# Optimization experiments

Hardware: AMD Instinct MI355X
Metric: run time of the kernel (lower is better)

The kernel has to match this reference:

```python
import jax, jax.numpy as jnp
import numpy as np

# Intersection(mode='product'):
#   a_fk = a @ feats.T            # [Na, K]
#   b_fk = b @ feats.T            # [Nb, K]
#   mask = (a_fk[:,None,:] > 0) & (b_fk[None,:,:] > 0)
#   result = sum_k (a_fk[:,None,:] * b_fk[None,:,:]) * mask   # [Na, Nb]
# For the product op, (x*y)*[x>0 & y>0] == relu(x)*relu(y) elementwise
# (any term with a non-positive factor is zeroed either way), so the
# broadcast+mask+reduce collapses exactly into a GEMM over relu'd scores.

def setup_inputs() -> dict:
    key = jax.random.key(0)
    k1, k2, k3 = jax.random.split(key, 3)
    a = jax.random.normal(k1, (1024, 2048), dtype=jnp.float32)
    b = jax.random.normal(k2, (1024, 2048), dtype=jnp.float32)
    feats = jax.random.normal(k3, (128, 2048), dtype=jnp.float32)
    return {"a": a, "b": b, "feats": feats}

def reference(a, b, feats):
    a_fk = a @ feats.T            # [Na, K]
    b_fk = b @ feats.T            # [Nb, K]
    # masked product-intersection reduced over K; identical math to the
    # broadcast (Na, Nb, K) -> sum formulation of the torch module.
    return jnp.einsum('ak,bk->ab', jax.nn.relu(a_fk), jax.nn.relu(b_fk))
```

## Files before the change

kernel.cpp:

```cpp
#include <hip/hip_runtime.h>


typedef __attribute__((ext_vector_type(8))) __bf16 bf16x8;
typedef __attribute__((ext_vector_type(4))) float floatx4;

#define KD     2048
#define NF     128
#define NA     1024
#define NPART  16

static __device__ inline bf16x8 cvt8(float4 u, float4 v) {
    bf16x8 s;
    s[0] = (__bf16)u.x; s[1] = (__bf16)u.y; s[2] = (__bf16)u.z; s[3] = (__bf16)u.w;
    s[4] = (__bf16)v.x; s[5] = (__bf16)v.y; s[6] = (__bf16)v.z; s[7] = (__bf16)v.w;
    return s;
}

static __device__ inline bf16x8 cvt8r(float4 u, float4 v) {
    bf16x8 s;
    s[0] = (__bf16)fmaxf(u.x, 0.f); s[1] = (__bf16)fmaxf(u.y, 0.f);
    s[2] = (__bf16)fmaxf(u.z, 0.f); s[3] = (__bf16)fmaxf(u.w, 0.f);
    s[4] = (__bf16)fmaxf(v.x, 0.f); s[5] = (__bf16)fmaxf(v.y, 0.f);
    s[6] = (__bf16)fmaxf(v.z, 0.f); s[7] = (__bf16)fmaxf(v.w, 0.f);
    return s;
}

__global__ __launch_bounds__(256) void gemm1_atomic(const float* __restrict__ A,
                                                    const float* __restrict__ B,
                                                    const float* __restrict__ F,
                                                    float* __restrict__ fk) {
    __shared__ __bf16 Xs[64 * 40];
    __shared__ __bf16 Fs[128 * 40];

    const int t    = threadIdx.x;
    const int m0   = blockIdx.x * 64;
    const int s    = blockIdx.y;
    const int k0   = s * 128;
    const float* src = (m0 < NA) ? (A + (size_t)m0 * KD)
                                 : (B + (size_t)(m0 - NA) * KD);

    const int lane = t & 63;
    const int w    = t >> 6;
    const int ln   = lane & 15;
    const int quad = lane >> 4;
    const int q8   = quad * 8;

    floatx4 acc[4][2];
#pragma unroll
    for (int mt = 0; mt < 4; mt++)
#pragma unroll
        for (int nt = 0; nt < 2; nt++)
            acc[mt][nt] = (floatx4){0.f, 0.f, 0.f, 0.f};

    const int xrow = t >> 2, xcol = (t & 3) * 8;
    const int frow = t >> 1, fcol = (t & 1) * 16;
    const float* xp = src + (size_t)xrow * KD + (k0 + xcol);
    const float* fp = F   + (size_t)frow * KD + (k0 + fcol);

    float4 xu = *(const float4*)(xp + 0);
    float4 xv = *(const float4*)(xp + 4);
    float4 f0 = *(const float4*)(fp + 0);
    float4 f1 = *(const float4*)(fp + 4);
    float4 f2 = *(const float4*)(fp + 8);
    float4 f3 = *(const float4*)(fp + 12);

#pragma unroll
    for (int kk = 0; kk < 128; kk += 32) {
        *(bf16x8*)&Xs[xrow * 40 + xcol]     = cvt8(xu, xv);
        *(bf16x8*)&Fs[frow * 40 + fcol]     = cvt8(f0, f1);
        *(bf16x8*)&Fs[frow * 40 + fcol + 8] = cvt8(f2, f3);
        __syncthreads();

        if (kk + 32 < 128) {
            xu = *(const float4*)(xp + kk + 32);
            xv = *(const float4*)(xp + kk + 36);
            f0 = *(const float4*)(fp + kk + 32);
            f1 = *(const float4*)(fp + kk + 36);
            f2 = *(const float4*)(fp + kk + 40);
            f3 = *(const float4*)(fp + kk + 44);
        }

        bf16x8 bfrag[2];
#pragma unroll
        for (int nt = 0; nt < 2; nt++)
            bfrag[nt] = *(const bf16x8*)&Fs[(w * 32 + nt * 16 + ln) * 40 + q8];
#pragma unroll
        for (int mt = 0; mt < 4; mt++) {
            bf16x8 af = *(const bf16x8*)&Xs[(mt * 16 + ln) * 40 + q8];
#pragma unroll
            for (int nt = 0; nt < 2; nt++)
                acc[mt][nt] = __builtin_amdgcn_mfma_f32_16x16x32_bf16(
                    af, bfrag[nt], acc[mt][nt], 0, 0, 0);
        }
        __syncthreads();
    }

#pragma unroll
    for (int mt = 0; mt < 4; mt++)
#pragma unroll
        for (int nt = 0; nt < 2; nt++)
#pragma unroll
            for (int r = 0; r < 4; r++) {
                int row = m0 + mt * 16 + quad * 4 + r;
                int col = w * 32 + nt * 16 + ln;
                atomicAdd(&fk[(size_t)row * NF + col], acc[mt][nt][r]);
            }
}

__global__ __launch_bounds__(256) void gemm2(const float* __restrict__ fk,
                                             float* __restrict__ out) {
    __shared__ __bf16 Ps[64 * 136];
    __shared__ __bf16 Qs[32 * 136];

    const int t    = threadIdx.x;
    const int i0   = blockIdx.y * 64;
    const int j0   = blockIdx.x * 32;
    const int lane = t & 63;
    const int w    = t >> 6;
    const int ln   = lane & 15;
    const int quad = lane >> 4;
    const int q8   = quad * 8;

    {
        const int prow = t >> 2, pcol = (t & 3) * 32;
        const float* p = fk + (size_t)(i0 + prow) * NF + pcol;
#pragma unroll
        for (int c = 0; c < 32; c += 8) {
            float4 u = *(const float4*)(p + c);
            float4 v = *(const float4*)(p + c + 4);
            *(bf16x8*)&Ps[prow * 136 + pcol + c] = cvt8r(u, v);
        }
    }
    {
        const int qrow = t >> 3, qcol = (t & 7) * 16;
        const float* q = fk + (size_t)(NA + j0 + qrow) * NF + qcol;
#pragma unroll
        for (int c = 0; c < 16; c += 8) {
            float4 u = *(const float4*)(q + c);
            float4 v = *(const float4*)(q + c + 4);
            *(bf16x8*)&Qs[qrow * 136 + qcol + c] = cvt8r(u, v);
        }
    }
    __syncthreads();

    const int wm = w & 1;
    const int wn = w >> 1;

    floatx4 acc2[2];
    acc2[0] = (floatx4){0.f, 0.f, 0.f, 0.f};
    acc2[1] = (floatx4){0.f, 0.f, 0.f, 0.f};

#pragma unroll
    for (int k0 = 0; k0 < 128; k0 += 32) {
        bf16x8 bfq = *(const bf16x8*)&Qs[(wn * 16 + ln) * 136 + k0 + q8];
#pragma unroll
        for (int mt = 0; mt < 2; mt++) {
            bf16x8 af = *(const bf16x8*)&Ps[(wm * 32 + mt * 16 + ln) * 136 + k0 + q8];
            acc2[mt] = __builtin_amdgcn_mfma_f32_16x16x32_bf16(
                af, bfq, acc2[mt], 0, 0, 0);
        }
    }

#pragma unroll
    for (int mt = 0; mt < 2; mt++)
#pragma unroll
        for (int r = 0; r < 4; r++) {
            int row = i0 + wm * 32 + mt * 16 + quad * 4 + r;
            int col = j0 + wn * 16 + ln;
            out[(size_t)row * 1024 + col] = acc2[mt][r];
        }
}

extern "C" void kernel_launch(void* const* d_in, const int* in_sizes, int n_in,
                              void* d_out, int out_size, void* d_ws, size_t ws_size,
                              hipStream_t stream) {
    const float* a     = (const float*)d_in[0];
    const float* b     = (const float*)d_in[1];
    const float* feats = (const float*)d_in[2];
    float* out = (float*)d_out;

    float* fk = (float*)d_ws;

    hipMemsetAsync(fk, 0, (size_t)2048 * NF * sizeof(float), stream);
    gemm1_atomic<<<dim3(32, NPART), 256, 0, stream>>>(a, b, feats, fk);
    gemm2<<<dim3(32, 16), 256, 0, stream>>>(fk, out);
}
```

Measured before the change: 88.72 us.

## Replace split-K atomic GEMM1 with full-K blocks writing relu'd bf16 scores

GEMM1 no longer splits K across 16 partitions with atomicAdd into a zeroed fp32 buffer. Each block now covers 32 rows over the full K=2048 and writes relu'd bf16 results directly, which removes the memset, the atomics and the conversion work in GEMM2. The cost is a grid of only 64 blocks on a GPU with many more CUs, each running a long serial K loop. That leaves most of the chip idle and makes each block stream F in full.

New measurement: 111.4 us. 25.6% more time.

```diff
diff --git a/kernel.cpp b/kernel.cpp
--- a/kernel.cpp
+++ b/kernel.cpp
@@ -2,12 +2,12 @@
 
 
 typedef __attribute__((ext_vector_type(8))) __bf16 bf16x8;
+typedef __attribute__((ext_vector_type(4))) __bf16 bf16x4;
 typedef __attribute__((ext_vector_type(4))) float floatx4;
 
 #define KD     2048
 #define NF     128
 #define NA     1024
-#define NPART  16
 
 static __device__ inline bf16x8 cvt8(float4 u, float4 v) {
     bf16x8 s;
@@ -16,26 +16,21 @@
     return s;
 }
 
-static __device__ inline bf16x8 cvt8r(float4 u, float4 v) {
-    bf16x8 s;
-    s[0] = (__bf16)fmaxf(u.x, 0.f); s[1] = (__bf16)fmaxf(u.y, 0.f);
-    s[2] = (__bf16)fmaxf(u.z, 0.f); s[3] = (__bf16)fmaxf(u.w, 0.f);
-    s[4] = (__bf16)fmaxf(v.x, 0.f); s[5] = (__bf16)fmaxf(v.y, 0.f);
-    s[6] = (__bf16)fmaxf(v.z, 0.f); s[7] = (__bf16)fmaxf(v.w, 0.f);
+static __device__ inline bf16x4 cvt4(float4 u) {
+    bf16x4 s;
+    s[0] = (__bf16)u.x; s[1] = (__bf16)u.y; s[2] = (__bf16)u.z; s[3] = (__bf16)u.w;
     return s;
 }
 
-__global__ __launch_bounds__(256) void gemm1_atomic(const float* __restrict__ A,
-                                                    const float* __restrict__ B,
-                                                    const float* __restrict__ F,
-                                                    float* __restrict__ fk) {
-    __shared__ __bf16 Xs[64 * 40];
+__global__ __launch_bounds__(256) void gemm1_full(const float* __restrict__ A,
+                                                  const float* __restrict__ B,
+                                                  const float* __restrict__ F,
+                                                  __bf16* __restrict__ fkb) {
+    __shared__ __bf16 Xs[32 * 40];
     __shared__ __bf16 Fs[128 * 40];
 
     const int t    = threadIdx.x;
-    const int m0   = blockIdx.x * 64;
-    const int s    = blockIdx.y;
-    const int k0   = s * 128;
+    const int m0   = blockIdx.x * 32;
     const float* src = (m0 < NA) ? (A + (size_t)m0 * KD)
                                  : (B + (size_t)(m0 - NA) * KD);
 
@@ -45,35 +40,33 @@
     const int quad = lane >> 4;
     const int q8   = quad * 8;
 
-    floatx4 acc[4][2];
+    floatx4 acc[2][2];
 #pragma unroll
-    for (int mt = 0; mt < 4; mt++)
+    for (int mt = 0; mt < 2; mt++)
 #pragma unroll
         for (int nt = 0; nt < 2; nt++)
             acc[mt][nt] = (floatx4){0.f, 0.f, 0.f, 0.f};
 
-    const int xrow = t >> 2, xcol = (t & 3) * 8;
+    const int xrow = t >> 3, xcol = (t & 7) * 4;
     const int frow = t >> 1, fcol = (t & 1) * 16;
-    const float* xp = src + (size_t)xrow * KD + (k0 + xcol);
-    const float* fp = F   + (size_t)frow * KD + (k0 + fcol);
+    const float* xp = src + (size_t)xrow * KD + xcol;
+    const float* fp = F   + (size_t)frow * KD + fcol;
 
     float4 xu = *(const float4*)(xp + 0);
-    float4 xv = *(const float4*)(xp + 4);
     float4 f0 = *(const float4*)(fp + 0);
     float4 f1 = *(const float4*)(fp + 4);
     float4 f2 = *(const float4*)(fp + 8);
     float4 f3 = *(const float4*)(fp + 12);
 
-#pragma unroll
-    for (int kk = 0; kk < 128; kk += 32) {
-        *(bf16x8*)&Xs[xrow * 40 + xcol]     = cvt8(xu, xv);
+#pragma unroll 4
+    for (int kk = 0; kk < KD; kk += 32) {
+        *(bf16x4*)&Xs[xrow * 40 + xcol]     = cvt4(xu);
         *(bf16x8*)&Fs[frow * 40 + fcol]     = cvt8(f0, f1);
         *(bf16x8*)&Fs[frow * 40 + fcol + 8] = cvt8(f2, f3);
         __syncthreads();
 
-        if (kk + 32 < 128) {
+        if (kk + 32 < KD) {
             xu = *(const float4*)(xp + kk + 32);
-            xv = *(const float4*)(xp + kk + 36);
             f0 = *(const float4*)(fp + kk + 32);
             f1 = *(const float4*)(fp + kk + 36);
             f2 = *(const float4*)(fp + kk + 40);
@@ -85,7 +78,7 @@
         for (int nt = 0; nt < 2; nt++)
             bfrag[nt] = *(const bf16x8*)&Fs[(w * 32 + nt * 16 + ln) * 40 + q8];
 #pragma unroll
-        for (int mt = 0; mt < 4; mt++) {
+        for (int mt = 0; mt < 2; mt++) {
             bf16x8 af = *(const bf16x8*)&Xs[(mt * 16 + ln) * 40 + q8];
 #pragma unroll
             for (int nt = 0; nt < 2; nt++)
@@ -96,18 +89,18 @@
     }
 
 #pragma unroll
-    for (int mt = 0; mt < 4; mt++)
+    for (int mt = 0; mt < 2; mt++)
 #pragma unroll
         for (int nt = 0; nt < 2; nt++)
 #pragma unroll
             for (int r = 0; r < 4; r++) {
                 int row = m0 + mt * 16 + quad * 4 + r;
                 int col = w * 32 + nt * 16 + ln;
-                atomicAdd(&fk[(size_t)row * NF + col], acc[mt][nt][r]);
+                fkb[(size_t)row * NF + col] = (__bf16)fmaxf(acc[mt][nt][r], 0.f);
             }
 }
 
-__global__ __launch_bounds__(256) void gemm2(const float* __restrict__ fk,
+__global__ __launch_bounds__(256) void gemm2(const __bf16* __restrict__ fkb,
                                              float* __restrict__ out) {
     __shared__ __bf16 Ps[64 * 136];
     __shared__ __bf16 Qs[32 * 136];
@@ -123,23 +116,17 @@
 
     {
         const int prow = t >> 2, pcol = (t & 3) * 32;
-        const float* p = fk + (size_t)(i0 + prow) * NF + pcol;
+        const __bf16* p = fkb + (size_t)(i0 + prow) * NF + pcol;
 #pragma unroll
-        for (int c = 0; c < 32; c += 8) {
-            float4 u = *(const float4*)(p + c);
-            float4 v = *(const float4*)(p + c + 4);
-            *(bf16x8*)&Ps[prow * 136 + pcol + c] = cvt8r(u, v);
-        }
+        for (int c = 0; c < 32; c += 8)
+            *(bf16x8*)&Ps[prow * 136 + pcol + c] = *(const bf16x8*)(p + c);
     }
     {
         const int qrow = t >> 3, qcol = (t & 7) * 16;
-        const float* q = fk + (size_t)(NA + j0 + qrow) * NF + qcol;
+        const __bf16* q = fkb + (size_t)(NA + j0 + qrow) * NF + qcol;
 #pragma unroll
-        for (int c = 0; c < 16; c += 8) {
-            float4 u = *(const float4*)(q + c);
-            float4 v = *(const float4*)(q + c + 4);
-            *(bf16x8*)&Qs[qrow * 136 + qcol + c] = cvt8r(u, v);
-        }
+        for (int c = 0; c < 16; c += 8)
+            *(bf16x8*)&Qs[qrow * 136 + qcol + c] = *(const bf16x8*)(q + c);
     }
     __syncthreads();
 
@@ -179,9 +166,8 @@
     const float* feats = (const float*)d_in[2];
     float* out = (float*)d_out;
 
-    float* fk = (float*)d_ws;
+    __bf16* fkb = (__bf16*)d_ws;
 
-    hipMemsetAsync(fk, 0, (size_t)2048 * NF * sizeof(float), stream);
-    gemm1_atomic<<<dim3(32, NPART), 256, 0, stream>>>(a, b, feats, fk);
-    gemm2<<<dim3(32, 16), 256, 0, stream>>>(fk, out);
+    gemm1_full<<<64, 256, 0, stream>>>(a, b, feats, fkb);
+    gemm2<<<dim3(32, 16), 256, 0, stream>>>(fkb, out);
 }
```
